# Kernel optimization log

Measured on AMD Instinct MI355X. Metric: run time of the kernel, lower is better.

Reference implementation:

```python
import jax, jax.numpy as jnp
import numpy as np

B, IMGS, PH, PW = 4, 4, 16, 16      # 4 groups, 4 images/group, 16x16 patches per image
P, C = 16, 3
N = IMGS * PH * PW                   # 1024 packed tokens per group
PATCH_DIM = C * P * P                # 768
DIM, HEADS, DHEAD, DEPTH = 768, 12, 64, 4
INNER = HEADS * DHEAD
MLP = 3072
POSMAX = 32                          # image_size // patch_size
NCLS = 1000
SCALE = DHEAD ** 0.5


def _ln(x, g):
    # torch LayerNorm with learned gamma, beta frozen at 0
    mu = jnp.mean(x, -1, keepdims=True)
    var = jnp.var(x, -1, keepdims=True)
    return (x - mu) * jax.lax.rsqrt(var + 1e-5) * g


def _qk_rmsnorm(t, g):
    # F.normalize(t, dim=-1) * sqrt(dhead) * gamma[h, 1, d]; t: (b,h,n,d), g: (h,d)
    nrm = jnp.sqrt(jnp.sum(t * t, -1, keepdims=True))
    return t / jnp.maximum(nrm, 1e-12) * SCALE * g[None, :, None, :]


def _attention(x, context, ln_g, Wq, Wkv, qg, kg, Wo, attn_mask):
    xn = _ln(x, ln_g)
    kv_in = xn if context is None else context  # context is NOT normed (matches torch)
    q = xn @ Wq
    k, v = jnp.split(kv_in @ Wkv, 2, axis=-1)
    split = lambda t: t.reshape(t.shape[0], t.shape[1], HEADS, DHEAD).transpose(0, 2, 1, 3)
    q, k, v = split(q), split(k), split(v)
    q = _qk_rmsnorm(q, qg)
    k = _qk_rmsnorm(k, kg)
    dots = jnp.einsum('bhid,bhjd->bhij', q, k)  # no 1/sqrt(d): scale lives in RMSNorm
    dots = jnp.where(attn_mask, dots, -jnp.finfo(dots.dtype).max)
    attn = jax.nn.softmax(dots, axis=-1)
    out = jnp.einsum('bhij,bhjd->bhid', attn, v)
    out = out.transpose(0, 2, 1, 3).reshape(x.shape[0], -1, INNER)
    return out @ Wo


def _forward(patches, emb_ln_g, W_emb, b_emb, emb_ln2_g, pos_h, pos_w,
             ln_attn_g, Wq, Wkv, qn_g, kn_g, Wo,
             ln_ff_g, W1, b1, W2, b2, final_ln_g,
             pool_q, pool_ln_g, pWq, pWkv, p_qn_g, p_kn_g, pWo,
             head_ln_g, W_head,
             patch_positions, image_ids, lengths):
    valid = jnp.arange(N)[None, :] < lengths[:, None]              # (B,N) True = real token
    same_img = image_ids[:, :, None] == image_ids[:, None, :]      # (B,i,j) block-diagonal
    attn_mask = (same_img & valid[:, None, :])[:, None]            # (B,1,i,j)

    x = _ln(patches, emb_ln_g) @ W_emb + b_emb
    x = _ln(x, emb_ln2_g)
    x = x + pos_h[patch_positions[..., 0]] + pos_w[patch_positions[..., 1]]

    for l in range(DEPTH):
        x = _attention(x, None, ln_attn_g[l], Wq[l], Wkv[l], qn_g[l], kn_g[l], Wo[l], attn_mask) + x
        h = jax.nn.gelu(_ln(x, ln_ff_g[l]) @ W1[l] + b1[l], approximate=False)
        x = h @ W2[l] + b2[l] + x
    x = _ln(x, final_ln_g)

    # attention pooling: one learned query per packed image
    queries = jnp.broadcast_to(pool_q, (x.shape[0], IMGS, DIM))
    pool_mask = ((jnp.arange(IMGS)[None, :, None] == image_ids[:, None, :]) & valid[:, None, :])[:, None]
    pooled = _attention(queries, x, pool_ln_g, pWq, pWkv, p_qn_g, p_kn_g, pWo, pool_mask) + queries
    return _ln(pooled, head_ln_g) @ W_head  # (B, IMGS, NCLS), mlp_head has no bias


def setup_inputs():
    key = jax.random.key(0)
    ks = jax.random.split(key, 20)
    rn = lambda k, shape, s=0.02: (jax.random.normal(k, shape) * s).astype(jnp.float32)

    patches = jax.random.normal(ks[0], (B, N, PATCH_DIM), dtype=jnp.float32)
    hh, ww = jnp.meshgrid(jnp.arange(PH), jnp.arange(PW), indexing='ij')
    pos = jnp.stack([hh.reshape(-1), ww.reshape(-1)], axis=-1)        # (256,2)
    patch_positions = jnp.broadcast_to(jnp.tile(pos, (IMGS, 1))[None], (B, N, 2)).astype(jnp.int32)
    image_ids = jnp.broadcast_to(jnp.repeat(jnp.arange(IMGS), PH * PW)[None], (B, N)).astype(jnp.int32)
    lengths = jnp.full((B,), N, dtype=jnp.int32)

    return dict(
        patches=patches, patch_positions=patch_positions, image_ids=image_ids, lengths=lengths,
        emb_ln_g=jnp.ones(PATCH_DIM, jnp.float32), W_emb=rn(ks[1], (PATCH_DIM, DIM)),
        b_emb=jnp.zeros(DIM, jnp.float32), emb_ln2_g=jnp.ones(DIM, jnp.float32),
        pos_h=rn(ks[2], (POSMAX, DIM), 1.0), pos_w=rn(ks[3], (POSMAX, DIM), 1.0),
        ln_attn_g=jnp.ones((DEPTH, DIM), jnp.float32),
        Wq=rn(ks[4], (DEPTH, DIM, INNER)), Wkv=rn(ks[5], (DEPTH, DIM, 2 * INNER)),
        qn_g=jnp.ones((DEPTH, HEADS, DHEAD), jnp.float32), kn_g=jnp.ones((DEPTH, HEADS, DHEAD), jnp.float32),
        Wo=rn(ks[6], (DEPTH, INNER, DIM)),
        ln_ff_g=jnp.ones((DEPTH, DIM), jnp.float32),
        W1=rn(ks[7], (DEPTH, DIM, MLP)), b1=jnp.zeros((DEPTH, MLP), jnp.float32),
        W2=rn(ks[8], (DEPTH, MLP, DIM)), b2=jnp.zeros((DEPTH, DIM), jnp.float32),
        final_ln_g=jnp.ones(DIM, jnp.float32),
        pool_q=rn(ks[9], (DIM,), 1.0), pool_ln_g=jnp.ones(DIM, jnp.float32),
        pWq=rn(ks[10], (DIM, INNER)), pWkv=rn(ks[11], (DIM, 2 * INNER)),
        p_qn_g=jnp.ones((HEADS, DHEAD), jnp.float32), p_kn_g=jnp.ones((HEADS, DHEAD), jnp.float32),
        pWo=rn(ks[12], (INNER, DIM)),
        head_ln_g=jnp.ones(DIM, jnp.float32), W_head=rn(ks[13], (DIM, NCLS)),
    )


def reference(patches, patch_positions, image_ids, lengths,
              emb_ln_g, W_emb, b_emb, emb_ln2_g, pos_h, pos_w,
              ln_attn_g, Wq, Wkv, qn_g, kn_g, Wo,
              ln_ff_g, W1, b1, W2, b2, final_ln_g,
              pool_q, pool_ln_g, pWq, pWkv, p_qn_g, p_kn_g, pWo,
              head_ln_g, W_head):
    return _forward(patches, emb_ln_g, W_emb, b_emb, emb_ln2_g, pos_h, pos_w,
                    ln_attn_g, Wq, Wkv, qn_g, kn_g, Wo,
                    ln_ff_g, W1, b1, W2, b2, final_ln_g,
                    pool_q, pool_ln_g, pWq, pWkv, p_qn_g, p_kn_g, pWo,
                    head_ln_g, W_head, patch_positions, image_ids, lengths)
```

## Files before the change

### kernel.cpp

```cpp
#include <hip/hip_runtime.h>
#include <hip/hip_bf16.h>
#include <math.h>

using bf16 = __hip_bfloat16;
typedef short s16x8 __attribute__((ext_vector_type(8)));
typedef short s16x4 __attribute__((ext_vector_type(4)));
typedef float f32x4 __attribute__((ext_vector_type(4)));

#define DEVI __device__ __forceinline__

static constexpr int NB    = 4;
static constexpr int NTOK  = 1024;
static constexpr int DIM   = 768;
static constexpr int NH    = 12;
static constexpr int MLPD  = 3072;
static constexpr int NLAYER= 4;
static constexpr int NIMG  = 4;
static constexpr int NCLS  = 1000;
static constexpr int MR    = NB * NTOK;
static constexpr size_t SLAB = (size_t)MR * 768;

DEVI float b2f(bf16 v){ return __bfloat162float(v); }
DEVI bf16  f2b(float v){ return __float2bfloat16(v); }
DEVI float bu2f(unsigned short u){ union{unsigned u32; float f;} w; w.u32 = ((unsigned)u)<<16; return w.f; }
DEVI unsigned short f2bu(float f){ bf16 b = f2b(f); return *(unsigned short*)&b; }

DEVI void async16(const void* g, void* l) {
  __builtin_amdgcn_global_load_lds((const __attribute__((address_space(1))) void*)g,
                                   (__attribute__((address_space(3))) void*)l, 16, 0, 0);
}

DEVI f32x4 mfma16(s16x8 a, s16x8 b, f32x4 c) {
  return __builtin_amdgcn_mfma_f32_16x16x32_bf16(a, b, c, 0, 0, 0);
}

template<int N> DEVI void waitcnt_vm() {
  if constexpr (N == 0)      asm volatile("s_waitcnt vmcnt(0)" ::: "memory");
  else if constexpr (N == 3) asm volatile("s_waitcnt vmcnt(3)" ::: "memory");
  else if constexpr (N == 4) asm volatile("s_waitcnt vmcnt(4)" ::: "memory");
  else if constexpr (N == 6) asm volatile("s_waitcnt vmcnt(6)" ::: "memory");
}

DEVI float block_sum(float v, float* scratch, int tid) {
  #pragma unroll
  for (int o = 32; o >= 1; o >>= 1) v += __shfl_xor(v, o);
  __syncthreads();
  if ((tid & 63) == 0) scratch[tid >> 6] = v;
  __syncthreads();
  return scratch[0] + scratch[1] + scratch[2] + scratch[3];
}

DEVI float block_max(float v, float* scratch, int tid) {
  #pragma unroll
  for (int o = 32; o >= 1; o >>= 1) v = fmaxf(v, __shfl_xor(v, o));
  __syncthreads();
  if ((tid & 63) == 0) scratch[tid >> 6] = v;
  __syncthreads();
  return fmaxf(fmaxf(scratch[0], scratch[1]), fmaxf(scratch[2], scratch[3]));
}

struct TEntry { const float* src; bf16* dst; int R, C, tiles, tC; };
struct TDesc  { TEntry e[22]; };

__global__ __launch_bounds__(256) void transpose_kernel(TDesc D, int nent) {
  int bid = blockIdx.x, ei = 0;
  while (ei < nent - 1 && bid >= D.e[ei].tiles) { bid -= D.e[ei].tiles; ++ei; }
  const TEntry E = D.e[ei];
  const int tr = bid / E.tC, tc = bid % E.tC;
  __shared__ unsigned short t[64][70];
  const int tid = threadIdx.x;
  {
    const int r = tid >> 4, c = (tid & 15) * 4;
    float4 v[4];
    #pragma unroll
    for (int p = 0; p < 4; ++p)
      v[p] = *(const float4*)(E.src + (size_t)(tr*64 + p*16 + r)*E.C + tc*64 + c);
    #pragma unroll
    for (int p = 0; p < 4; ++p) {
      unsigned short* dst = &t[p*16 + r][c];
      dst[0] = f2bu(v[p].x); dst[1] = f2bu(v[p].y); dst[2] = f2bu(v[p].z); dst[3] = f2bu(v[p].w);
    }
  }
  __syncthreads();
  #pragma unroll
  for (int p = 0; p < 2; ++p) {
    const int n = p*32 + (tid >> 3);
    const int r0 = (tid & 7) * 8;
    s16x8 o;
    #pragma unroll
    for (int i = 0; i < 8; ++i) o[i] = (short)t[r0 + i][n];
    *(s16x8*)((short*)E.dst + (size_t)(tc*64 + n)*E.R + tr*64 + r0) = o;
  }
}

__global__ __launch_bounds__(256) void ln768_kernel(const float* __restrict__ in,
    const float* __restrict__ g, bf16* __restrict__ out)
{
  __shared__ float scratch[4];
  const int row = blockIdx.x, tid = threadIdx.x;
  const float* p = in + (size_t)row*768;
  const float v0 = p[tid], v1 = p[tid+256], v2 = p[tid+512];
  const float s  = block_sum(v0+v1+v2, scratch, tid);
  const float ss = block_sum(v0*v0+v1*v1+v2*v2, scratch, tid);
  const float mu = s * (1.0f/768.0f);
  const float var = ss * (1.0f/768.0f) - mu*mu;
  const float rstd = rsqrtf(var + 1e-5f);
  bf16* o = out + (size_t)row*768;
  o[tid]     = f2b((v0-mu)*rstd*g[tid]);
  o[tid+256] = f2b((v1-mu)*rstd*g[tid+256]);
  o[tid+512] = f2b((v2-mu)*rstd*g[tid+512]);
}

template<int HAS_BIAS>
__global__ __launch_bounds__(256) void res2_ln_kernel(float* __restrict__ x,
    const float* __restrict__ P, const float* __restrict__ bias,
    const float* __restrict__ g, bf16* __restrict__ xn)
{
  __shared__ float scratch[4];
  const int row = blockIdx.x, tid = threadIdx.x;
  const size_t base = (size_t)row*768;
  const float* p0 = P + base;
  const float* p1 = P + SLAB + base;
  float* xr = x + base;
  float v[3];
  #pragma unroll
  for (int i = 0; i < 3; ++i) {
    const int c = tid + i*256;
    float t = xr[c] + p0[c] + p1[c];
    if constexpr (HAS_BIAS) t += bias[c];
    v[i] = t;
    xr[c] = t;
  }
  const float s  = block_sum(v[0]+v[1]+v[2], scratch, tid);
  const float ss = block_sum(v[0]*v[0]+v[1]*v[1]+v[2]*v[2], scratch, tid);
  const float mu = s * (1.0f/768.0f);
  const float rstd = rsqrtf(ss*(1.0f/768.0f) - mu*mu + 1e-5f);
  bf16* o = xn + base;
  #pragma unroll
  for (int i = 0; i < 3; ++i) {
    const int c = tid + i*256;
    o[c] = f2b((v[i]-mu)*rstd*g[c]);
  }
}

__global__ __launch_bounds__(256) void ln_pos2_kernel(const float* __restrict__ P,
    const float* __restrict__ bias, const float* __restrict__ g,
    const float* __restrict__ pos_h, const float* __restrict__ pos_w,
    const int* __restrict__ ppos, float* __restrict__ out,
    const float* __restrict__ g2, bf16* __restrict__ xn)
{
  __shared__ float scratch[4];
  const int row = blockIdx.x, tid = threadIdx.x;
  const size_t base = (size_t)row*768;
  const float* p0 = P + base;
  const float* p1 = P + SLAB + base;
  float v[3];
  #pragma unroll
  for (int i = 0; i < 3; ++i) {
    const int c = tid + i*256;
    v[i] = p0[c] + p1[c] + bias[c];
  }
  const float s  = block_sum(v[0]+v[1]+v[2], scratch, tid);
  const float ss = block_sum(v[0]*v[0]+v[1]*v[1]+v[2]*v[2], scratch, tid);
  const float mu = s * (1.0f/768.0f);
  const float rstd = rsqrtf(ss*(1.0f/768.0f) - mu*mu + 1e-5f);
  const int p0i = ppos[row*2], p1i = ppos[row*2+1];
  const float* ph = pos_h + (size_t)p0i*768;
  const float* pw = pos_w + (size_t)p1i*768;
  float* o = out + base;
  float xv[3];
  #pragma unroll
  for (int i = 0; i < 3; ++i) {
    const int c = tid + i*256;
    xv[i] = (v[i]-mu)*rstd*g[c] + ph[c] + pw[c];
    o[c] = xv[i];
  }
  const float s2  = block_sum(xv[0]+xv[1]+xv[2], scratch, tid);
  const float ss2 = block_sum(xv[0]*xv[0]+xv[1]*xv[1]+xv[2]*xv[2], scratch, tid);
  const float mu2 = s2 * (1.0f/768.0f);
  const float rstd2 = rsqrtf(ss2*(1.0f/768.0f) - mu2*mu2 + 1e-5f);
  bf16* on = xn + base;
  #pragma unroll
  for (int i = 0; i < 3; ++i) {
    const int c = tid + i*256;
    on[c] = f2b((xv[i]-mu2)*rstd2*g2[c]);
  }
}

template<int DO_BIAS, int DO_GELU, int OUT_BF16, int DO_RES, int NTILE, int SPLITK, int RMSQKV>
__global__ __launch_bounds__(256)
void gemm_mfma(const bf16* __restrict__ A, const bf16* __restrict__ BT,
               const float* __restrict__ bias, float* __restrict__ Cf,
               bf16* __restrict__ Cb,
               const float* __restrict__ qg, const float* __restrict__ kg,
               bf16* __restrict__ Qp, bf16* __restrict__ Kp, bf16* __restrict__ Vp,
               int M, int Nn, int K)
{
  constexpr int NF  = NTILE / 32;
  constexpr int PD  = 3;
  constexpr int LPI = 2 + NTILE/64;
  constexpr int VW  = (PD - 2) * LPI;
  __shared__ bf16 As[PD][64*64];
  __shared__ bf16 Bs[PD][(NTILE/2)*64];
  const int tid = threadIdx.x;
  const int wid = tid >> 6, lane = tid & 63;
  const int quad = lane >> 4, l15 = lane & 15;
  const int wy = wid >> 1, wx = wid & 1;

  const int gx  = gridDim.x;
  const int nwg = gx * gridDim.y;
  const int bid = blockIdx.y * gx + blockIdx.x;
  const int qq  = nwg >> 3, rm = nwg & 7;
  const int xcd = bid & 7,  li = bid >> 3;
  const int swz = (xcd < rm ? xcd * (qq + 1) : rm * (qq + 1) + (xcd - rm) * qq) + li;
  const int m0 = (swz / gx) * 128, n0 = (swz % gx) * NTILE;

  const int kz    = (SPLITK > 1) ? blockIdx.z : 0;
  const int kloc  = K / SPLITK;
  const int kbase = kz * kloc;

  const int rl = lane >> 3;
  const int cs = lane & 7;

  f32x4 acc[4][NF];
  #pragma unroll
  for (int i = 0; i < 4; ++i)
    #pragma unroll
    for (int j = 0; j < NF; ++j) acc[i][j] = (f32x4){0.f,0.f,0.f,0.f};

  auto stage = [&](int buf, int k0) {
    #pragma unroll
    for (int c = 0; c < 2; ++c) {
      const int rbase = wid*8 + c*32;
      const int r_abs = rbase + rl;
      const int ceff  = cs ^ (r_abs & 7);
      const int mg    = 2*r_abs + (ceff >> 2);
      const int jb    = (ceff & 3) * 16;
      async16((const char*)A + ((size_t)(m0 + mg)*K + k0)*2 + jb, (char*)As[buf] + rbase*128);
    }
    #pragma unroll
    for (int c = 0; c < NTILE/64; ++c) {
      const int rbase = wid*8 + c*32;
      const int r_abs = rbase + rl;
      const int ceff  = cs ^ (r_abs & 7);
      const int ng    = 2*r_abs + (ceff >> 2);
      const int jb    = (ceff & 3) * 16;
      async16((const char*)BT + ((size_t)(n0 + ng)*K + k0)*2 + jb, (char*)Bs[buf] + rbase*128);
    }
  };

  auto compute = [&](int cb) {
    s16x8 af[4], bfr[NF];
    #pragma unroll
    for (int mt = 0; mt < 4; ++mt) {
      const int m = wy*64 + mt*16 + l15;
      const int r = m >> 1;
      const int cq = (((m & 1) << 2) | quad) ^ (r & 7);
      af[mt] = *(const s16x8*)((const char*)As[cb] + r*128 + cq*16);
    }
    #pragma unroll
    for (int nt = 0; nt < NF; ++nt) {
      const int n = wx*(NTILE/2) + nt*16 + l15;
      const int r = n >> 1;
      const int cq = (((n & 1) << 2) | quad) ^ (r & 7);
      bfr[nt] = *(const s16x8*)((const char*)Bs[cb] + r*128 + cq*16);
    }
    #pragma unroll
    for (int mt = 0; mt < 4; ++mt)
      #pragma unroll
      for (int nt = 0; nt < NF; ++nt)
        acc[mt][nt] = mfma16(af[mt], bfr[nt], acc[mt][nt]);
  };

  const int nk = kloc >> 5;
  #pragma unroll
  for (int t = 0; t < PD - 1; ++t) stage(t, kbase + (t << 5));

  int cbuf = 0, sbuf = PD - 1;
  const int mainN = nk - (PD - 1);
  for (int kt = 0; kt < mainN; ++kt) {
    __builtin_amdgcn_sched_barrier(0);
    waitcnt_vm<VW>();
    __builtin_amdgcn_s_barrier();
    __builtin_amdgcn_sched_barrier(0);
    stage(sbuf, kbase + ((kt + PD - 1) << 5));
    compute(cbuf);
    cbuf = (cbuf + 1 == PD) ? 0 : cbuf + 1;
    sbuf = (sbuf + 1 == PD) ? 0 : sbuf + 1;
  }
  for (int kt = mainN; kt < nk; ++kt) {
    __builtin_amdgcn_sched_barrier(0);
    waitcnt_vm<0>();
    __builtin_amdgcn_s_barrier();
    __builtin_amdgcn_sched_barrier(0);
    compute(cbuf);
    cbuf = (cbuf + 1 == PD) ? 0 : cbuf + 1;
  }

  if constexpr (RMSQKV) {
    const int hslice = (n0 >> 6) + wx;
    const int region = hslice / NH;
    const int h  = hslice - region*NH;
    const int b  = m0 >> 10;
    const int bh = b*NH + h;
    const int tokb = m0 & (NTOK-1);
    if (region < 2) {
      const float* gp = (region == 0) ? (qg + h*64) : (kg + h*64);
      bf16* outb = (region == 0) ? Qp : Kp;
      #pragma unroll
      for (int mt = 0; mt < 4; ++mt)
        #pragma unroll
        for (int rr = 0; rr < 4; ++rr) {
          float ssq = 0.f;
          #pragma unroll
          for (int nt = 0; nt < NF; ++nt) ssq += acc[mt][nt][rr]*acc[mt][nt][rr];
          #pragma unroll
          for (int o = 1; o <= 8; o <<= 1) ssq += __shfl_xor(ssq, o);
          const float rn = 8.0f / fmaxf(sqrtf(ssq), 1e-12f);
          const int tok = tokb + wy*64 + mt*16 + quad*4 + rr;
          #pragma unroll
          for (int nt = 0; nt < NF; ++nt) {
            const int d = nt*16 + l15;
            outb[((size_t)bh*NTOK + tok)*64 + d] = f2b(acc[mt][nt][rr]*rn*gp[d]);
          }
        }
    } else {
      #pragma unroll
      for (int mt = 0; mt < 4; ++mt)
        #pragma unroll
        for (int nt = 0; nt < NF; ++nt) {
          const int d = nt*16 + l15;
          const int tok = tokb + wy*64 + mt*16 + quad*4;
          s16x4 pk;
          #pragma unroll
          for (int rr = 0; rr < 4; ++rr) pk[rr] = (short)f2bu(acc[mt][nt][rr]);
          *(s16x4*)((short*)Vp + ((size_t)bh*64 + d)*NTOK + tok) = pk;
        }
    }
  } else {
    float* Cslab = (SPLITK > 1) ? (Cf + (size_t)kz * SLAB) : Cf;
    #pragma unroll
    for (int nt = 0; nt < NF; ++nt) {
      const int col = n0 + wx*(NTILE/2) + nt*16 + l15;
      float bv = 0.f;
      if constexpr (DO_BIAS) bv = bias[col];
      #pragma unroll
      for (int mt = 0; mt < 4; ++mt) {
        #pragma unroll
        for (int r = 0; r < 4; ++r) {
          const int row = m0 + wy*64 + mt*16 + quad*4 + r;
          float v = acc[mt][nt][r];
          if constexpr (DO_BIAS) v += bv;
          if constexpr (DO_GELU) v = 0.5f*v*(1.0f + erff(v*0.70710678118654752f));
          const size_t idx = (size_t)row*Nn + col;
          if constexpr (OUT_BF16) Cb[idx] = f2b(v);
          else if constexpr (DO_RES) Cf[idx] += v;
          else Cslab[idx] = v;
        }
      }
    }
  }
}

template<int IN_BF16, int DO_BIAS>
__global__ __launch_bounds__(256) void smallm_gemm(const void* __restrict__ Xv,
    const float* __restrict__ W, const float* __restrict__ bias,
    float* __restrict__ out, int Nn)
{
  __shared__ float Xs[16*768];
  __shared__ float red[4][16][64];
  const int tid = threadIdx.x;
  if constexpr (IN_BF16) {
    const bf16* X = (const bf16*)Xv;
    for (int i = tid; i < 16*768; i += 256) Xs[i] = b2f(X[i]);
  } else {
    const float* X = (const float*)Xv;
    for (int i = tid; i < 16*768; i += 256) Xs[i] = X[i];
  }
  __syncthreads();
  const int cl = tid & 63, kg = tid >> 6;
  const int c = blockIdx.x*64 + cl;
  float acc[16];
  #pragma unroll
  for (int r = 0; r < 16; ++r) acc[r] = 0.f;
  if (c < Nn) {
    const int k0 = kg*192;
    #pragma unroll 4
    for (int k = k0; k < k0 + 192; ++k) {
      const float w = W[(size_t)k*Nn + c];
      #pragma unroll
      for (int r = 0; r < 16; ++r) acc[r] += Xs[r*768 + k] * w;
    }
  }
  #pragma unroll
  for (int r = 0; r < 16; ++r) red[kg][r][cl] = acc[r];
  __syncthreads();
  if (kg == 0 && c < Nn) {
    #pragma unroll
    for (int r = 0; r < 16; ++r) {
      float v = red[0][r][cl] + red[1][r][cl] + red[2][r][cl] + red[3][r][cl];
      if constexpr (DO_BIAS) v += bias[c];
      out[(size_t)r*Nn + c] = v;
    }
  }
}

__global__ __launch_bounds__(256) void attn_mfma(const bf16* __restrict__ Qb,
    const bf16* __restrict__ Kb, const bf16* __restrict__ VTb, bf16* __restrict__ Ob,
    const int* __restrict__ ids, const int* __restrict__ lens)
{
  __shared__ bf16 Ps[4][16*72];
  __shared__ int  ids_s[NTOK];
  const int qt = blockIdx.x, h = blockIdx.y, b = blockIdx.z;
  const int tid = threadIdx.x;
  const int wid = tid >> 6, lane = tid & 63;
  const int quad = lane >> 4, l15 = lane & 15;
  const int bh = b*NH + h;
  const int q0 = qt*64;
  const int len = lens[b];

  #pragma unroll
  for (int i = 0; i < 4; ++i) ids_s[i*256 + tid] = ids[b*NTOK + i*256 + tid];
  __syncthreads();

  const bf16* qrow = Qb + ((size_t)bh*NTOK + q0 + wid*16 + l15)*64;
  const s16x8 aq0 = *(const s16x8*)(qrow + quad*8);
  const s16x8 aq1 = *(const s16x8*)(qrow + 32 + quad*8);

  int idq[4];
  #pragma unroll
  for (int rr = 0; rr < 4; ++rr) idq[rr] = ids_s[q0 + wid*16 + quad*4 + rr];

  unsigned qm = 0;
  #pragma unroll
  for (int rr = 0; rr < 4; ++rr) qm |= 1u << (idq[rr] & 31);
  #pragma unroll
  for (int o = 32; o >= 1; o >>= 1) qm |= (unsigned)__shfl_xor((int)qm, o);

  f32x4 oacc[4];
  #pragma unroll
  for (int nt = 0; nt < 4; ++nt) oacc[nt] = (f32x4){0.f,0.f,0.f,0.f};
  float mrow[4] = {-3.0e38f,-3.0e38f,-3.0e38f,-3.0e38f};
  float lrow[4] = {0.f,0.f,0.f,0.f};

  const bf16* Kgb = Kb  + (size_t)bh*NTOK*64;
  const bf16* Vgb = VTb + (size_t)bh*64*NTOK;
  bf16* pw = Ps[wid];

  for (int kt = 0; kt < 16; ++kt) {
    const int k0 = kt*64;
    const int idk_l = ids_s[k0 + lane];
    const bool ok = ((k0 + lane) < len) && (((qm >> (idk_l & 31)) & 1u) != 0u);
    if (__ballot(ok) == 0ULL) continue;

    f32x4 sA[4];
    #pragma unroll
    for (int jt = 0; jt < 4; ++jt) {
      const bf16* krow = Kgb + (size_t)(k0 + jt*16 + l15)*64;
      const s16x8 bk0 = *(const s16x8*)(krow + quad*8);
      const s16x8 bk1 = *(const s16x8*)(krow + 32 + quad*8);
      f32x4 s = (f32x4){0.f,0.f,0.f,0.f};
      s = mfma16(aq0, bk0, s);
      s = mfma16(aq1, bk1, s);
      sA[jt] = s;
    }
    #pragma unroll
    for (int jt = 0; jt < 4; ++jt) {
      const int j = k0 + jt*16 + l15;
      const int idk = ids_s[j];
      const bool kvld = j < len;
      #pragma unroll
      for (int rr = 0; rr < 4; ++rr)
        sA[jt][rr] = (kvld && idk == idq[rr]) ? sA[jt][rr] : -3.0e38f;
    }
    float alpha[4], mnew[4];
    #pragma unroll
    for (int rr = 0; rr < 4; ++rr) {
      float mx = fmaxf(fmaxf(sA[0][rr], sA[1][rr]), fmaxf(sA[2][rr], sA[3][rr]));
      mx = fmaxf(mx, __shfl_xor(mx, 1));
      mx = fmaxf(mx, __shfl_xor(mx, 2));
      mx = fmaxf(mx, __shfl_xor(mx, 4));
      mx = fmaxf(mx, __shfl_xor(mx, 8));
      const float mn = fmaxf(mrow[rr], mx);
      mnew[rr] = mn;
      alpha[rr] = expf(mrow[rr] - mn);
      mrow[rr] = mn;
    }
    #pragma unroll
    for (int rr = 0; rr < 4; ++rr) {
      float rs = 0.f;
      #pragma unroll
      for (int jt = 0; jt < 4; ++jt) {
        const float pv = (sA[jt][rr] > -1.0e38f) ? expf(sA[jt][rr] - mnew[rr]) : 0.0f;
        sA[jt][rr] = pv;
        rs += pv;
      }
      rs += __shfl_xor(rs, 1);
      rs += __shfl_xor(rs, 2);
      rs += __shfl_xor(rs, 4);
      rs += __shfl_xor(rs, 8);
      lrow[rr] = lrow[rr]*alpha[rr] + rs;
      #pragma unroll
      for (int nt = 0; nt < 4; ++nt) oacc[nt][rr] *= alpha[rr];
    }
    #pragma unroll
    for (int jt = 0; jt < 4; ++jt)
      #pragma unroll
      for (int rr = 0; rr < 4; ++rr)
        pw[(quad*4+rr)*72 + jt*16 + l15] = f2b(sA[jt][rr]);
    #pragma unroll
    for (int ss = 0; ss < 2; ++ss) {
      const s16x8 ap = *(const s16x8*)(pw + l15*72 + ss*32 + quad*8);
      #pragma unroll
      for (int nt = 0; nt < 4; ++nt) {
        const s16x8 bv = *(const s16x8*)(Vgb + (size_t)(nt*16 + l15)*NTOK + k0 + ss*32 + quad*8);
        oacc[nt] = mfma16(ap, bv, oacc[nt]);
      }
    }
  }

  #pragma unroll
  for (int rr = 0; rr < 4; ++rr) {
    const float inv = lrow[rr] > 0.f ? 1.0f/lrow[rr] : 0.0f;
    const int n = q0 + wid*16 + quad*4 + rr;
    bf16* orow = Ob + ((size_t)b*NTOK + n)*768 + h*64;
    #pragma unroll
    for (int nt = 0; nt < 4; ++nt)
      orow[nt*16 + l15] = f2b(oacc[nt][rr]*inv);
  }
}

__global__ __launch_bounds__(256) void pool_q_kernel(const float* __restrict__ pool_q,
    const float* __restrict__ pool_ln_g, const float* __restrict__ pWq,
    const float* __restrict__ p_qn_g, float* __restrict__ qp)
{
  __shared__ float xn[768];
  __shared__ float scratch[4];
  __shared__ float qraw[64];
  const int h = blockIdx.x, tid = threadIdx.x;
  float v0 = pool_q[tid], v1 = pool_q[tid+256], v2 = pool_q[tid+512];
  const float s  = block_sum(v0+v1+v2, scratch, tid);
  const float ss = block_sum(v0*v0+v1*v1+v2*v2, scratch, tid);
  const float mu = s*(1.0f/768.0f);
  const float rstd = rsqrtf(ss*(1.0f/768.0f) - mu*mu + 1e-5f);
  xn[tid]     = (v0-mu)*rstd*pool_ln_g[tid];
  xn[tid+256] = (v1-mu)*rstd*pool_ln_g[tid+256];
  xn[tid+512] = (v2-mu)*rstd*pool_ln_g[tid+512];
  __syncthreads();
  const int d = tid >> 2, pp = tid & 3;
  const int col = h*64 + d;
  float acc = 0.f;
  for (int k = pp*192; k < (pp+1)*192; ++k) acc += xn[k]*pWq[(size_t)k*768 + col];
  acc += __shfl_xor(acc, 1); acc += __shfl_xor(acc, 2);
  if (pp == 0) qraw[d] = acc;
  __syncthreads();
  if (tid < 64) {
    const float q = qraw[tid];
    float sq = q*q;
    #pragma unroll
    for (int o = 32; o >= 1; o >>= 1) sq += __shfl_xor(sq, o);
    const float rn = 8.0f / fmaxf(sqrtf(sq), 1e-12f);
    qp[h*64 + tid] = q * rn * p_qn_g[h*64 + tid];
  }
}

__global__ __launch_bounds__(256) void pool_attn_kernel(const bf16* __restrict__ kvp,
    const float* __restrict__ qp, const float* __restrict__ kg,
    const int* __restrict__ ids, const int* __restrict__ lens, float* __restrict__ pooled)
{
  __shared__ float sp[1024];
  __shared__ float qg_s[64];
  __shared__ float scratch[4];
  __shared__ float outred[4][64];
  const int h = blockIdx.x, img = blockIdx.y, b = blockIdx.z;
  const int tid = threadIdx.x;
  const int len = lens[b];
  if (tid < 64) qg_s[tid] = qp[h*64 + tid] * kg[h*64 + tid];
  __syncthreads();

  float smax = -3.0e38f;
  for (int j = tid; j < 1024; j += 256) {
    float sv = -3.0e38f;
    if (j < len && ids[b*NTOK + j] == img) {
      const bf16* kr = kvp + (size_t)(b*NTOK + j)*1536 + h*64;
      float ssq = 0.f, dq = 0.f;
      #pragma unroll
      for (int dd = 0; dd < 64; dd += 8) {
        s16x8 k8 = *(const s16x8*)(kr + dd);
        #pragma unroll
        for (int i = 0; i < 8; ++i) {
          const float kv = bu2f((unsigned short)k8[i]);
          ssq += kv*kv;
          dq  += qg_s[dd+i]*kv;
        }
      }
      const float rn = 8.0f / fmaxf(sqrtf(ssq), 1e-12f);
      sv = dq * rn;
    }
    sp[j] = sv;
    smax = fmaxf(smax, sv);
  }
  const float M = block_max(smax, scratch, tid);
  float lsum = 0.f;
  for (int j = tid; j < 1024; j += 256) {
    const float p = (sp[j] > -1.0e38f) ? expf(sp[j] - M) : 0.0f;
    sp[j] = p;
    lsum += p;
  }
  const float L = block_sum(lsum, scratch, tid);
  const float invL = L > 0.f ? 1.0f / L : 0.0f;

  const int d = tid & 63, jg = tid >> 6;
  float acc = 0.f;
  for (int j = jg; j < 1024; j += 4) {
    const float p = sp[j];
    if (p > 0.f) acc += p * b2f(kvp[(size_t)(b*NTOK + j)*1536 + 768 + h*64 + d]);
  }
  outred[jg][d] = acc;
  __syncthreads();
  if (tid < 64) {
    const float o = (outred[0][tid] + outred[1][tid] + outred[2][tid] + outred[3][tid]) * invL;
    pooled[((size_t)b*NIMG + img)*768 + h*64 + tid] = o;
  }
}

extern "C" void kernel_launch(void* const* d_in, const int* in_sizes, int n_in,
                              void* d_out, int out_size, void* d_ws, size_t ws_size,
                              hipStream_t stream)
{
  const float* patches    = (const float*)d_in[0];
  const int*   ppos       = (const int*)d_in[1];
  const int*   image_ids  = (const int*)d_in[2];
  const int*   lengths    = (const int*)d_in[3];
  const float* emb_ln_g   = (const float*)d_in[4];
  const float* W_emb      = (const float*)d_in[5];
  const float* b_emb      = (const float*)d_in[6];
  const float* emb_ln2_g  = (const float*)d_in[7];
  const float* pos_h      = (const float*)d_in[8];
  const float* pos_w      = (const float*)d_in[9];
  const float* ln_attn_g  = (const float*)d_in[10];
  const float* Wq         = (const float*)d_in[11];
  const float* Wkv        = (const float*)d_in[12];
  const float* qn_g       = (const float*)d_in[13];
  const float* kn_g       = (const float*)d_in[14];
  const float* Wo         = (const float*)d_in[15];
  const float* ln_ff_g    = (const float*)d_in[16];
  const float* W1         = (const float*)d_in[17];
  const float* b1         = (const float*)d_in[18];
  const float* W2         = (const float*)d_in[19];
  const float* b2v        = (const float*)d_in[20];
  const float* final_ln_g = (const float*)d_in[21];
  const float* pool_q     = (const float*)d_in[22];
  const float* pool_ln_g  = (const float*)d_in[23];
  const float* pWq        = (const float*)d_in[24];
  const float* pWkv       = (const float*)d_in[25];
  const float* p_qn_g     = (const float*)d_in[26];
  const float* p_kn_g     = (const float*)d_in[27];
  const float* pWo        = (const float*)d_in[28];
  const float* head_ln_g  = (const float*)d_in[29];
  const float* W_head     = (const float*)d_in[30];

  char* ws = (char*)d_ws;
  size_t off = 0;
  auto alloc = [&](size_t sz){ size_t r = off; off += (sz + 255) & ~(size_t)255; return r; };

  const size_t o_WembT = alloc((size_t)768*768*2);
  size_t o_QKVT[4], o_WoT[4], o_W1T[4], o_W2T[4];
  for (int l = 0; l < NLAYER; ++l) {
    o_QKVT[l] = alloc((size_t)2304*768*2);
    o_WoT[l]  = alloc((size_t)768*768*2);
    o_W1T[l]  = alloc((size_t)3072*768*2);
    o_W2T[l]  = alloc((size_t)768*3072*2);
  }
  const size_t o_pWkvT = alloc((size_t)1536*768*2);
  const size_t o_x     = alloc((size_t)MR*768*4);
  const size_t o_xn    = alloc((size_t)MR*768*2);
  const size_t o_kv    = alloc((size_t)MR*3072*2);
  const size_t o_P     = alloc((size_t)2*SLAB*4);
  const size_t o_Qb    = alloc((size_t)MR*768*2);
  const size_t o_Kb    = alloc((size_t)MR*768*2);
  const size_t o_VT    = alloc((size_t)MR*768*2);
  const size_t o_Ob    = alloc((size_t)MR*768*2);
  const size_t o_qp    = alloc((size_t)768*4);
  const size_t o_pool  = alloc((size_t)16*768*4);
  const size_t o_poolf = alloc((size_t)16*768*4);
  const size_t o_hl    = alloc((size_t)16*768*2);
  if (off > ws_size) return;

  float* x    = (float*)(ws + o_x);
  bf16*  xn   = (bf16*)(ws + o_xn);
  bf16*  hb   = (bf16*)(ws + o_kv);
  bf16*  kvb  = (bf16*)(ws + o_kv);
  float* P    = (float*)(ws + o_P);
  bf16*  Qb   = (bf16*)(ws + o_Qb);
  bf16*  Kb   = (bf16*)(ws + o_Kb);
  bf16*  VTb  = (bf16*)(ws + o_VT);
  bf16*  Ob   = (bf16*)(ws + o_Ob);
  float* qp   = (float*)(ws + o_qp);
  float* pooled  = (float*)(ws + o_pool);
  float* pooledf = (float*)(ws + o_poolf);
  bf16*  hl   = (bf16*)(ws + o_hl);

  TDesc td; int ne = 0, total = 0;
  auto add = [&](const float* s, size_t dofs, int R, int C){
    td.e[ne].src = s;
    td.e[ne].dst = (bf16*)(ws + dofs);
    td.e[ne].R = R; td.e[ne].C = C;
    td.e[ne].tiles = (R/64)*(C/64); td.e[ne].tC = C/64;
    total += td.e[ne].tiles; ++ne;
  };
  add(W_emb, o_WembT, 768, 768);
  for (int l = 0; l < NLAYER; ++l) {
    add(Wq  + (size_t)l*768*768,  o_QKVT[l],                 768, 768);
    add(Wkv + (size_t)l*768*1536, o_QKVT[l] + (size_t)768*768*2, 768, 1536);
    add(Wo  + (size_t)l*768*768,  o_WoT[l],                  768, 768);
    add(W1  + (size_t)l*768*3072, o_W1T[l],                  768, 3072);
    add(W2  + (size_t)l*3072*768, o_W2T[l],                  3072, 768);
  }
  add(pWkv, o_pWkvT, 768, 1536);
  transpose_kernel<<<total, 256, 0, stream>>>(td, ne);

  ln768_kernel<<<MR, 256, 0, stream>>>(patches, emb_ln_g, xn);
  gemm_mfma<0,0,0,0,64,2,0><<<dim3(12,32,2), 256, 0, stream>>>(xn, (const bf16*)(ws+o_WembT), nullptr,
      P, nullptr, nullptr, nullptr, nullptr, nullptr, nullptr, MR, 768, 768);
  ln_pos2_kernel<<<MR, 256, 0, stream>>>(P, b_emb, emb_ln2_g, pos_h, pos_w, ppos, x, ln_attn_g, xn);

  for (int l = 0; l < NLAYER; ++l) {
    gemm_mfma<0,0,0,0,128,1,1><<<dim3(18,32), 256, 0, stream>>>(xn, (const bf16*)(ws+o_QKVT[l]), nullptr,
        nullptr, nullptr, qn_g + (size_t)l*768, kn_g + (size_t)l*768, Qb, Kb, VTb, MR, 2304, 768);
    attn_mfma<<<dim3(16,NH,NB), 256, 0, stream>>>(Qb, Kb, VTb, Ob, image_ids, lengths);
    gemm_mfma<0,0,0,0,64,2,0><<<dim3(12,32,2), 256, 0, stream>>>(Ob, (const bf16*)(ws+o_WoT[l]), nullptr,
        P, nullptr, nullptr, nullptr, nullptr, nullptr, nullptr, MR, 768, 768);
    res2_ln_kernel<0><<<MR, 256, 0, stream>>>(x, P, nullptr, ln_ff_g + (size_t)l*768, xn);
    gemm_mfma<1,1,1,0,128,1,0><<<dim3(24,32), 256, 0, stream>>>(xn, (const bf16*)(ws+o_W1T[l]), b1 + (size_t)l*3072,
        nullptr, hb, nullptr, nullptr, nullptr, nullptr, nullptr, MR, 3072, 768);
    gemm_mfma<0,0,0,0,64,2,0><<<dim3(12,32,2), 256, 0, stream>>>(hb, (const bf16*)(ws+o_W2T[l]), nullptr,
        P, nullptr, nullptr, nullptr, nullptr, nullptr, nullptr, MR, 768, 3072);
    const float* gnext = (l + 1 < NLAYER) ? (ln_attn_g + (size_t)(l+1)*768) : final_ln_g;
    res2_ln_kernel<1><<<MR, 256, 0, stream>>>(x, P, b2v + (size_t)l*768, gnext, xn);
  }

  gemm_mfma<0,0,1,0,64,1,0><<<dim3(24,32), 256, 0, stream>>>(xn, (const bf16*)(ws+o_pWkvT), nullptr,
      nullptr, kvb, nullptr, nullptr, nullptr, nullptr, nullptr, MR, 1536, 768);
  pool_q_kernel<<<NH, 256, 0, stream>>>(pool_q, pool_ln_g, pWq, p_qn_g, qp);
  pool_attn_kernel<<<dim3(NH,NIMG,NB), 256, 0, stream>>>(kvb, qp, p_kn_g, image_ids, lengths, pooled);
  smallm_gemm<0,1><<<12, 256, 0, stream>>>(pooled, pWo, pool_q, pooledf, 768);
  ln768_kernel<<<16, 256, 0, stream>>>(pooledf, head_ln_g, hl);
  smallm_gemm<1,0><<<16, 256, 0, stream>>>(hl, W_head, nullptr, (float*)d_out, NCLS);
}
```

Baseline: 1.105 ms.

## Parameterize GEMM waves and pipeline depth; use 8 waves for wide tiles, batch transposes

The MFMA GEMM gets WAVES and PD template parameters. The QKV and FFN1 GEMMs (128-wide N tiles) now run with 512 threads, so each wave owns fewer M rows, while the 64-wide GEMMs use a 4-deep LDS pipeline. The weight-transpose kernel now handles two 64x64 tiles per block, halving the launched grid. The aim is more latency hiding and occupancy in the main GEMMs, at the cost of LDS usage, register pressure and wait-count tuning.

Result: faster. 1.013 ms (-8.3%).

```diff
diff --git a/kernel.cpp b/kernel.cpp
--- a/kernel.cpp
+++ b/kernel.cpp
@@ -36,6 +36,7 @@
 
 template<int N> DEVI void waitcnt_vm() {
   if constexpr (N == 0)      asm volatile("s_waitcnt vmcnt(0)" ::: "memory");
+  else if constexpr (N == 2) asm volatile("s_waitcnt vmcnt(2)" ::: "memory");
   else if constexpr (N == 3) asm volatile("s_waitcnt vmcnt(3)" ::: "memory");
   else if constexpr (N == 4) asm volatile("s_waitcnt vmcnt(4)" ::: "memory");
   else if constexpr (N == 6) asm volatile("s_waitcnt vmcnt(6)" ::: "memory");
@@ -63,33 +64,39 @@
 struct TDesc  { TEntry e[22]; };
 
 __global__ __launch_bounds__(256) void transpose_kernel(TDesc D, int nent) {
-  int bid = blockIdx.x, ei = 0;
-  while (ei < nent - 1 && bid >= D.e[ei].tiles) { bid -= D.e[ei].tiles; ++ei; }
+  int tix = blockIdx.x * 2, ei = 0;
+  while (ei < nent - 1 && tix >= D.e[ei].tiles) { tix -= D.e[ei].tiles; ++ei; }
   const TEntry E = D.e[ei];
-  const int tr = bid / E.tC, tc = bid % E.tC;
-  __shared__ unsigned short t[64][70];
+  __shared__ unsigned short t[2][64][70];
   const int tid = threadIdx.x;
-  {
-    const int r = tid >> 4, c = (tid & 15) * 4;
-    float4 v[4];
+  const int r = tid >> 4, c = (tid & 15) * 4;
+  float4 v[2][4];
+  #pragma unroll
+  for (int q = 0; q < 2; ++q) {
+    const int tr = (tix + q) / E.tC, tc = (tix + q) % E.tC;
     #pragma unroll
     for (int p = 0; p < 4; ++p)
-      v[p] = *(const float4*)(E.src + (size_t)(tr*64 + p*16 + r)*E.C + tc*64 + c);
+      v[q][p] = *(const float4*)(E.src + (size_t)(tr*64 + p*16 + r)*E.C + tc*64 + c);
+  }
+  #pragma unroll
+  for (int q = 0; q < 2; ++q) {
     #pragma unroll
     for (int p = 0; p < 4; ++p) {
-      unsigned short* dst = &t[p*16 + r][c];
-      dst[0] = f2bu(v[p].x); dst[1] = f2bu(v[p].y); dst[2] = f2bu(v[p].z); dst[3] = f2bu(v[p].w);
-    }
-  }
-  __syncthreads();
-  #pragma unroll
-  for (int p = 0; p < 2; ++p) {
-    const int n = p*32 + (tid >> 3);
-    const int r0 = (tid & 7) * 8;
-    s16x8 o;
-    #pragma unroll
-    for (int i = 0; i < 8; ++i) o[i] = (short)t[r0 + i][n];
-    *(s16x8*)((short*)E.dst + (size_t)(tc*64 + n)*E.R + tr*64 + r0) = o;
+      unsigned short* dst = &t[q][p*16 + r][c];
+      dst[0] = f2bu(v[q][p].x); dst[1] = f2bu(v[q][p].y);
+      dst[2] = f2bu(v[q][p].z); dst[3] = f2bu(v[q][p].w);
+    }
+    __syncthreads();
+    const int tr = (tix + q) / E.tC, tc = (tix + q) % E.tC;
+    #pragma unroll
+    for (int p = 0; p < 2; ++p) {
+      const int n = p*32 + (tid >> 3);
+      const int r0 = (tid & 7) * 8;
+      s16x8 o;
+      #pragma unroll
+      for (int i = 0; i < 8; ++i) o[i] = (short)t[q][r0 + i][n];
+      *(s16x8*)((short*)E.dst + (size_t)(tc*64 + n)*E.R + tr*64 + r0) = o;
+    }
   }
 }
 
@@ -187,8 +194,9 @@
   }
 }
 
-template<int DO_BIAS, int DO_GELU, int OUT_BF16, int DO_RES, int NTILE, int SPLITK, int RMSQKV>
-__global__ __launch_bounds__(256)
+template<int DO_BIAS, int DO_GELU, int OUT_BF16, int DO_RES, int NTILE, int SPLITK,
+         int RMSQKV, int WAVES, int PD>
+__global__ __launch_bounds__(WAVES*64)
 void gemm_mfma(const bf16* __restrict__ A, const bf16* __restrict__ BT,
                const float* __restrict__ bias, float* __restrict__ Cf,
                bf16* __restrict__ Cb,
@@ -196,10 +204,14 @@
                bf16* __restrict__ Qp, bf16* __restrict__ Kp, bf16* __restrict__ Vp,
                int M, int Nn, int K)
 {
-  constexpr int NF  = NTILE / 32;
-  constexpr int PD  = 3;
-  constexpr int LPI = 2 + NTILE/64;
-  constexpr int VW  = (PD - 2) * LPI;
+  constexpr int NF    = NTILE / 32;
+  constexpr int WY    = WAVES / 2;
+  constexpr int MROWS = 128 / WY;
+  constexpr int MF    = MROWS / 16;
+  constexpr int ALOOPS = 64 / (8*WAVES);
+  constexpr int BLOOPS = (NTILE/2) / (8*WAVES);
+  constexpr int LPI   = ALOOPS + BLOOPS;
+  constexpr int VW    = (PD - 2) * LPI;
   __shared__ bf16 As[PD][64*64];
   __shared__ bf16 Bs[PD][(NTILE/2)*64];
   const int tid = threadIdx.x;
@@ -222,16 +234,16 @@
   const int rl = lane >> 3;
   const int cs = lane & 7;
 
-  f32x4 acc[4][NF];
-  #pragma unroll
-  for (int i = 0; i < 4; ++i)
+  f32x4 acc[MF][NF];
+  #pragma unroll
+  for (int i = 0; i < MF; ++i)
     #pragma unroll
     for (int j = 0; j < NF; ++j) acc[i][j] = (f32x4){0.f,0.f,0.f,0.f};
 
   auto stage = [&](int buf, int k0) {
     #pragma unroll
-    for (int c = 0; c < 2; ++c) {
-      const int rbase = wid*8 + c*32;
+    for (int c = 0; c < ALOOPS; ++c) {
+      const int rbase = wid*8 + c*(8*WAVES);
       const int r_abs = rbase + rl;
       const int ceff  = cs ^ (r_abs & 7);
       const int mg    = 2*r_abs + (ceff >> 2);
@@ -239,8 +251,8 @@
       async16((const char*)A + ((size_t)(m0 + mg)*K + k0)*2 + jb, (char*)As[buf] + rbase*128);
     }
     #pragma unroll
-    for (int c = 0; c < NTILE/64; ++c) {
-      const int rbase = wid*8 + c*32;
+    for (int c = 0; c < BLOOPS; ++c) {
+      const int rbase = wid*8 + c*(8*WAVES);
       const int r_abs = rbase + rl;
       const int ceff  = cs ^ (r_abs & 7);
       const int ng    = 2*r_abs + (ceff >> 2);
@@ -250,10 +262,10 @@
   };
 
   auto compute = [&](int cb) {
-    s16x8 af[4], bfr[NF];
-    #pragma unroll
-    for (int mt = 0; mt < 4; ++mt) {
-      const int m = wy*64 + mt*16 + l15;
+    s16x8 af[MF], bfr[NF];
+    #pragma unroll
+    for (int mt = 0; mt < MF; ++mt) {
+      const int m = wy*MROWS + mt*16 + l15;
       const int r = m >> 1;
       const int cq = (((m & 1) << 2) | quad) ^ (r & 7);
       af[mt] = *(const s16x8*)((const char*)As[cb] + r*128 + cq*16);
@@ -266,7 +278,7 @@
       bfr[nt] = *(const s16x8*)((const char*)Bs[cb] + r*128 + cq*16);
     }
     #pragma unroll
-    for (int mt = 0; mt < 4; ++mt)
+    for (int mt = 0; mt < MF; ++mt)
       #pragma unroll
       for (int nt = 0; nt < NF; ++nt)
         acc[mt][nt] = mfma16(af[mt], bfr[nt], acc[mt][nt]);
@@ -308,7 +320,7 @@
       const float* gp = (region == 0) ? (qg + h*64) : (kg + h*64);
       bf16* outb = (region == 0) ? Qp : Kp;
       #pragma unroll
-      for (int mt = 0; mt < 4; ++mt)
+      for (int mt = 0; mt < MF; ++mt)
         #pragma unroll
         for (int rr = 0; rr < 4; ++rr) {
           float ssq = 0.f;
@@ -317,7 +329,7 @@
           #pragma unroll
           for (int o = 1; o <= 8; o <<= 1) ssq += __shfl_xor(ssq, o);
           const float rn = 8.0f / fmaxf(sqrtf(ssq), 1e-12f);
-          const int tok = tokb + wy*64 + mt*16 + quad*4 + rr;
+          const int tok = tokb + wy*MROWS + mt*16 + quad*4 + rr;
           #pragma unroll
           for (int nt = 0; nt < NF; ++nt) {
             const int d = nt*16 + l15;
@@ -326,11 +338,11 @@
         }
     } else {
       #pragma unroll
-      for (int mt = 0; mt < 4; ++mt)
+      for (int mt = 0; mt < MF; ++mt)
         #pragma unroll
         for (int nt = 0; nt < NF; ++nt) {
           const int d = nt*16 + l15;
-          const int tok = tokb + wy*64 + mt*16 + quad*4;
+          const int tok = tokb + wy*MROWS + mt*16 + quad*4;
           s16x4 pk;
           #pragma unroll
           for (int rr = 0; rr < 4; ++rr) pk[rr] = (short)f2bu(acc[mt][nt][rr]);
@@ -345,16 +357,16 @@
       float bv = 0.f;
       if constexpr (DO_BIAS) bv = bias[col];
       #pragma unroll
-      for (int mt = 0; mt < 4; ++mt) {
+      for (int mt = 0; mt < MF; ++mt) {
         #pragma unroll
         for (int r = 0; r < 4; ++r) {
-          const int row = m0 + wy*64 + mt*16 + quad*4 + r;
+          const int row = m0 + wy*MROWS + mt*16 + quad*4 + r;
           float v = acc[mt][nt][r];
           if constexpr (DO_BIAS) v += bv;
           if constexpr (DO_GELU) v = 0.5f*v*(1.0f + erff(v*0.70710678118654752f));
           const size_t idx = (size_t)row*Nn + col;
           if constexpr (OUT_BF16) Cb[idx] = f2b(v);
-          else if constexpr (DO_RES) Cf[idx] += v;
+          else if constexpr (DO_RES) Cslab[idx] += v;
           else Cslab[idx] = v;
         }
       }
@@ -718,29 +730,29 @@
     add(W2  + (size_t)l*3072*768, o_W2T[l],                  3072, 768);
   }
   add(pWkv, o_pWkvT, 768, 1536);
-  transpose_kernel<<<total, 256, 0, stream>>>(td, ne);
+  transpose_kernel<<<total/2, 256, 0, stream>>>(td, ne);
 
   ln768_kernel<<<MR, 256, 0, stream>>>(patches, emb_ln_g, xn);
-  gemm_mfma<0,0,0,0,64,2,0><<<dim3(12,32,2), 256, 0, stream>>>(xn, (const bf16*)(ws+o_WembT), nullptr,
+  gemm_mfma<0,0,0,0,64,2,0,4,4><<<dim3(12,32,2), 256, 0, stream>>>(xn, (const bf16*)(ws+o_WembT), nullptr,
       P, nullptr, nullptr, nullptr, nullptr, nullptr, nullptr, MR, 768, 768);
   ln_pos2_kernel<<<MR, 256, 0, stream>>>(P, b_emb, emb_ln2_g, pos_h, pos_w, ppos, x, ln_attn_g, xn);
 
   for (int l = 0; l < NLAYER; ++l) {
-    gemm_mfma<0,0,0,0,128,1,1><<<dim3(18,32), 256, 0, stream>>>(xn, (const bf16*)(ws+o_QKVT[l]), nullptr,
+    gemm_mfma<0,0,0,0,128,1,1,8,3><<<dim3(18,32), 512, 0, stream>>>(xn, (const bf16*)(ws+o_QKVT[l]), nullptr,
         nullptr, nullptr, qn_g + (size_t)l*768, kn_g + (size_t)l*768, Qb, Kb, VTb, MR, 2304, 768);
     attn_mfma<<<dim3(16,NH,NB), 256, 0, stream>>>(Qb, Kb, VTb, Ob, image_ids, lengths);
-    gemm_mfma<0,0,0,0,64,2,0><<<dim3(12,32,2), 256, 0, stream>>>(Ob, (const bf16*)(ws+o_WoT[l]), nullptr,
+    gemm_mfma<0,0,0,0,64,2,0,4,4><<<dim3(12,32,2), 256, 0, stream>>>(Ob, (const bf16*)(ws+o_WoT[l]), nullptr,
         P, nullptr, nullptr, nullptr, nullptr, nullptr, nullptr, MR, 768, 768);
     res2_ln_kernel<0><<<MR, 256, 0, stream>>>(x, P, nullptr, ln_ff_g + (size_t)l*768, xn);
-    gemm_mfma<1,1,1,0,128,1,0><<<dim3(24,32), 256, 0, stream>>>(xn, (const bf16*)(ws+o_W1T[l]), b1 + (size_t)l*3072,
+    gemm_mfma<1,1,1,0,128,1,0,8,3><<<dim3(24,32), 512, 0, stream>>>(xn, (const bf16*)(ws+o_W1T[l]), b1 + (size_t)l*3072,
         nullptr, hb, nullptr, nullptr, nullptr, nullptr, nullptr, MR, 3072, 768);
-    gemm_mfma<0,0,0,0,64,2,0><<<dim3(12,32,2), 256, 0, stream>>>(hb, (const bf16*)(ws+o_W2T[l]), nullptr,
+    gemm_mfma<0,0,0,0,64,2,0,4,4><<<dim3(12,32,2), 256, 0, stream>>>(hb, (const bf16*)(ws+o_W2T[l]), nullptr,
         P, nullptr, nullptr, nullptr, nullptr, nullptr, nullptr, MR, 768, 3072);
     const float* gnext = (l + 1 < NLAYER) ? (ln_attn_g + (size_t)(l+1)*768) : final_ln_g;
     res2_ln_kernel<1><<<MR, 256, 0, stream>>>(x, P, b2v + (size_t)l*768, gnext, xn);
   }
 
-  gemm_mfma<0,0,1,0,64,1,0><<<dim3(24,32), 256, 0, stream>>>(xn, (const bf16*)(ws+o_pWkvT), nullptr,
+  gemm_mfma<0,0,1,0,64,1,0,4,4><<<dim3(24,32), 256, 0, stream>>>(xn, (const bf16*)(ws+o_pWkvT), nullptr,
       nullptr, kvb, nullptr, nullptr, nullptr, nullptr, nullptr, MR, 1536, 768);
   pool_q_kernel<<<NH, 256, 0, stream>>>(pool_q, pool_ln_g, pWq, p_qn_g, qp);
   pool_attn_kernel<<<dim3(NH,NIMG,NB), 256, 0, stream>>>(kvb, qp, p_kn_g, image_ids, lengths, pooled);
```
